# Kernel optimization log

Measured on AMD Instinct MI355X. Metric: run time of the kernel, lower is better.

## Reference

```python
import jax, jax.numpy as jnp
import numpy as np

D = 8        # num_decoders
N = 65536    # num_entries
LAT = 64     # latent_dim
HID = 128    # hidden_dim_dec
FEAT = 16    # feature_dim


def setup_inputs() -> dict:
    key = jax.random.key(0)
    ks = jax.random.split(key, 6)
    return {
        "weight": jax.random.normal(ks[0], (N, LAT), jnp.float32) * 2.0,
        "alpha_param": jax.random.normal(ks[1], (D, N), jnp.float32),  # alpha_std=1.0
        "div": jnp.ones((LAT,), jnp.float32),
        "scale0": jax.random.normal(ks[2], (D, LAT, HID), jnp.float32),  # ldec_std=1.0 normal init
        "shift0": jnp.zeros((D, 1, HID), jnp.float32),
        "scale1": jax.random.normal(ks[3], (D, HID, HID), jnp.float32),
        "shift1": jnp.zeros((D, 1, HID), jnp.float32),
        "scale2": jax.random.normal(ks[4], (D, HID, FEAT), jnp.float32),
        "shift2": jnp.zeros((D, 1, FEAT), jnp.float32),
    }


def _st_round(x):
    # StraightThrough: round in forward, identity gradient
    return x + jax.lax.stop_gradient(jnp.round(x) - x)


def _layer(x, alpha, scale, shift):
    # x: [N, I], alpha: [D, N], scale: [D, I, O], shift: [D, 1, O]
    out = jnp.einsum('ni,dio->dno', x, scale)           # per-decoder GEMMs [D,N,O]
    mix = jnp.einsum('dno,dn->no', out, alpha)          # alpha-weighted combine
    # second alpha-weighted sum over (mix + per-decoder shift), as in the torch code
    return jnp.einsum('dno,dn->no', mix[None, :, :] + shift, alpha)


def reference(weight, alpha_param, div, scale0, shift0, scale1, shift1, scale2, shift2):
    temperature = 1.0
    a = jax.nn.softmax(alpha_param / temperature, axis=0)       # [D, N]
    idx = jnp.argmax(a, axis=0)                                 # [N]
    onehot = jax.nn.one_hot(idx, a.shape[0], dtype=a.dtype).T   # [D, N]
    alpha = a + jax.lax.stop_gradient(onehot - a)               # straight-through one-hot

    x = _st_round(weight) / div                                 # [N, LAT]
    x = jax.nn.relu(_layer(x, alpha, scale0, shift0))           # [N, HID]
    x = jax.nn.relu(_layer(x, alpha, scale1, shift1))           # [N, HID]
    out = _layer(x, alpha, scale2, shift2)                      # [N, FEAT], final_activation='none'
    return out
```

## Files before the change

### kernel.cpp

```cpp
#include <hip/hip_runtime.h>

#define NN 65536
#define DD 8
#define LATD 64
#define HIDD 128
#define FEATD 16
#define BPD 96
#define SXS 72
#define SHS 136

typedef __attribute__((ext_vector_type(8))) short short8;
typedef __attribute__((ext_vector_type(4))) float f32x4;
typedef __attribute__((ext_vector_type(8))) unsigned short ushort8;

static __device__ __forceinline__ unsigned short f2bf(float f) {
  union { float f; unsigned u; } v; v.f = f;
  unsigned r = v.u + 0x7FFFu + ((v.u >> 16) & 1u);
  return (unsigned short)(r >> 16);
}

__global__ __launch_bounds__(256) void k_prep(
    const float* __restrict__ ap, int* __restrict__ cursor,
    unsigned short* __restrict__ perm,
    const float* __restrict__ s0, const float* __restrict__ s1,
    const float* __restrict__ s2,
    unsigned short* __restrict__ g0, unsigned short* __restrict__ g1,
    unsigned short* __restrict__ g2) {
  int bid = blockIdx.x;
  int t = threadIdx.x;
  if (bid < 256) {
    __shared__ int bc[DD];
    __shared__ int bbase[DD];
    if (t < DD) bc[t] = 0;
    __syncthreads();
    int n = bid * 256 + t;
    float best = ap[n];
    int bd = 0;
#pragma unroll
    for (int d = 1; d < DD; ++d) {
      float v = ap[d * NN + n];
      if (v > best) { best = v; bd = d; }
    }
    int lr = atomicAdd(&bc[bd], 1);
    __syncthreads();
    if (t < DD) bbase[t] = atomicAdd(&cursor[t], bc[t]);
    __syncthreads();
    perm[bd * NN + bbase[bd] + lr] = (unsigned short)n;
  } else {
    int o = (bid - 256) * 256 + t;
    if (o < DD * HIDD * LATD) {
      int d = o >> 13, rem = o & 8191, n = rem >> 6, k = rem & 63;
      g0[o] = f2bf(s0[d * 8192 + k * 128 + n]);
    }
    if (o < DD * HIDD * HIDD) {
      int d = o >> 14, rem = o & 16383, n = rem >> 7, k = rem & 127;
      g1[o] = f2bf(s1[d * 16384 + k * 128 + n]);
    }
    if (o < DD * FEATD * HIDD) {
      int d = o >> 11, rem = o & 2047, n = rem >> 7, k = rem & 127;
      g2[o] = f2bf(s2[d * 2048 + k * 16 + n]);
    }
  }
}

__global__ __launch_bounds__(256, 3) void k_mlp(
    const float* __restrict__ weight, const float* __restrict__ divv,
    const unsigned short* __restrict__ g0, const float* __restrict__ sh0,
    const unsigned short* __restrict__ g1, const float* __restrict__ sh1,
    const unsigned short* __restrict__ g2, const float* __restrict__ sh2,
    const int* __restrict__ cursor, const unsigned short* __restrict__ perm,
    float* __restrict__ out) {
  __shared__ unsigned short sX[64 * SXS];
  __shared__ unsigned short sH1[64 * SHS];
  __shared__ unsigned short sH2[64 * SHS];
  __shared__ unsigned short sP[64];

  int d = blockIdx.x / BPD, bslot = blockIdx.x % BPD;
  int cnt = cursor[d];
  int t = threadIdx.x;
  int w = t >> 6, l = t & 63;
  int lrow = l & 15, kgrp = l >> 4;

  short8 b0[2][2];
  short8 b1[2][4];
  short8 b2[4];
  float sh0v[2], sh1v[2];
  const unsigned short* G0 = g0 + d * (HIDD * LATD);
  const unsigned short* G1 = g1 + d * (HIDD * HIDD);
  const unsigned short* G2 = g2 + d * (FEATD * HIDD);
#pragma unroll
  for (int cb = 0; cb < 2; ++cb) {
    int n = (2 * w + cb) * 16 + lrow;
#pragma unroll
    for (int ks = 0; ks < 2; ++ks)
      b0[cb][ks] = *(const short8*)&G0[n * LATD + ks * 32 + kgrp * 8];
#pragma unroll
    for (int ks = 0; ks < 4; ++ks)
      b1[cb][ks] = *(const short8*)&G1[n * HIDD + ks * 32 + kgrp * 8];
    sh0v[cb] = sh0[d * HIDD + n];
    sh1v[cb] = sh1[d * HIDD + n];
  }
#pragma unroll
  for (int ks = 0; ks < 4; ++ks)
    b2[ks] = *(const short8*)&G2[lrow * HIDD + ks * 32 + kgrp * 8];
  float sh2v = sh2[d * FEATD + lrow];

  for (int tile = bslot; tile * 64 < cnt; tile += BPD) {
    int base = tile * 64;

    {
      int r = t >> 2, c = t & 3;
      int gp = base + r;
      unsigned short pe = 0;
      short8 lo = {0, 0, 0, 0, 0, 0, 0, 0}, hi = {0, 0, 0, 0, 0, 0, 0, 0};
      if (gp < cnt) {
        pe = perm[d * NN + gp];
        const float* wr = weight + (int)pe * LATD + c * 16;
        const float* dv = divv + c * 16;
#pragma unroll
        for (int q = 0; q < 2; ++q) {
          float4 f = *(const float4*)(wr + q * 4);
          float4 g = *(const float4*)(dv + q * 4);
          lo[q * 4 + 0] = (short)f2bf(rintf(f.x) / g.x);
          lo[q * 4 + 1] = (short)f2bf(rintf(f.y) / g.y);
          lo[q * 4 + 2] = (short)f2bf(rintf(f.z) / g.z);
          lo[q * 4 + 3] = (short)f2bf(rintf(f.w) / g.w);
        }
#pragma unroll
        for (int q = 0; q < 2; ++q) {
          float4 f = *(const float4*)(wr + 8 + q * 4);
          float4 g = *(const float4*)(dv + 8 + q * 4);
          hi[q * 4 + 0] = (short)f2bf(rintf(f.x) / g.x);
          hi[q * 4 + 1] = (short)f2bf(rintf(f.y) / g.y);
          hi[q * 4 + 2] = (short)f2bf(rintf(f.z) / g.z);
          hi[q * 4 + 3] = (short)f2bf(rintf(f.w) / g.w);
        }
      }
      if (c == 0) sP[r] = pe;
      *(short8*)&sX[r * SXS + c * 16] = lo;
      *(short8*)&sX[r * SXS + c * 16 + 8] = hi;
    }
    __syncthreads();

    int prow[4];
#pragma unroll
    for (int rr = 0; rr < 4; ++rr) prow[rr] = (int)sP[w * 16 + kgrp * 4 + rr];

#pragma unroll
    for (int rg = 0; rg < 4; ++rg) {
      short8 a0 = *(short8*)&sX[(rg * 16 + lrow) * SXS + kgrp * 8];
      short8 a1 = *(short8*)&sX[(rg * 16 + lrow) * SXS + 32 + kgrp * 8];
      __builtin_amdgcn_s_setprio(1);
#pragma unroll
      for (int cb = 0; cb < 2; ++cb) {
        f32x4 acc = {sh0v[cb], sh0v[cb], sh0v[cb], sh0v[cb]};
        acc = __builtin_amdgcn_mfma_f32_16x16x32_bf16(a0, b0[cb][0], acc, 0, 0, 0);
        acc = __builtin_amdgcn_mfma_f32_16x16x32_bf16(a1, b0[cb][1], acc, 0, 0, 0);
#pragma unroll
        for (int rr = 0; rr < 4; ++rr)
          sH1[(rg * 16 + kgrp * 4 + rr) * SHS + (2 * w + cb) * 16 + lrow] =
              f2bf(fmaxf(acc[rr], 0.f));
      }
      __builtin_amdgcn_s_setprio(0);
    }
    __syncthreads();

#pragma unroll
    for (int rg = 0; rg < 4; ++rg) {
      short8 h0 = *(short8*)&sH1[(rg * 16 + lrow) * SHS + kgrp * 8];
      short8 h1 = *(short8*)&sH1[(rg * 16 + lrow) * SHS + 32 + kgrp * 8];
      short8 h2 = *(short8*)&sH1[(rg * 16 + lrow) * SHS + 64 + kgrp * 8];
      short8 h3 = *(short8*)&sH1[(rg * 16 + lrow) * SHS + 96 + kgrp * 8];
      __builtin_amdgcn_s_setprio(1);
#pragma unroll
      for (int cb = 0; cb < 2; ++cb) {
        f32x4 acc = {sh1v[cb], sh1v[cb], sh1v[cb], sh1v[cb]};
        acc = __builtin_amdgcn_mfma_f32_16x16x32_bf16(h0, b1[cb][0], acc, 0, 0, 0);
        acc = __builtin_amdgcn_mfma_f32_16x16x32_bf16(h1, b1[cb][1], acc, 0, 0, 0);
        acc = __builtin_amdgcn_mfma_f32_16x16x32_bf16(h2, b1[cb][2], acc, 0, 0, 0);
        acc = __builtin_amdgcn_mfma_f32_16x16x32_bf16(h3, b1[cb][3], acc, 0, 0, 0);
#pragma unroll
        for (int rr = 0; rr < 4; ++rr)
          sH2[(rg * 16 + kgrp * 4 + rr) * SHS + (2 * w + cb) * 16 + lrow] =
              f2bf(fmaxf(acc[rr], 0.f));
      }
      __builtin_amdgcn_s_setprio(0);
    }
    __syncthreads();

    {
      short8 q0 = *(short8*)&sH2[(w * 16 + lrow) * SHS + kgrp * 8];
      short8 q1 = *(short8*)&sH2[(w * 16 + lrow) * SHS + 32 + kgrp * 8];
      short8 q2 = *(short8*)&sH2[(w * 16 + lrow) * SHS + 64 + kgrp * 8];
      short8 q3 = *(short8*)&sH2[(w * 16 + lrow) * SHS + 96 + kgrp * 8];
      f32x4 acc = {sh2v, sh2v, sh2v, sh2v};
      __builtin_amdgcn_s_setprio(1);
      acc = __builtin_amdgcn_mfma_f32_16x16x32_bf16(q0, b2[0], acc, 0, 0, 0);
      acc = __builtin_amdgcn_mfma_f32_16x16x32_bf16(q1, b2[1], acc, 0, 0, 0);
      acc = __builtin_amdgcn_mfma_f32_16x16x32_bf16(q2, b2[2], acc, 0, 0, 0);
      acc = __builtin_amdgcn_mfma_f32_16x16x32_bf16(q3, b2[3], acc, 0, 0, 0);
      __builtin_amdgcn_s_setprio(0);
#pragma unroll
      for (int rr = 0; rr < 4; ++rr) {
        int row = w * 16 + kgrp * 4 + rr;
        if (base + row < cnt) out[prow[rr] * FEATD + lrow] = acc[rr];
      }
    }
  }
}

extern "C" void kernel_launch(void* const* d_in, const int* in_sizes, int n_in,
                              void* d_out, int out_size, void* d_ws, size_t ws_size,
                              hipStream_t stream) {
  const float* weight      = (const float*)d_in[0];
  const float* alpha_param = (const float*)d_in[1];
  const float* divv        = (const float*)d_in[2];
  const float* scale0      = (const float*)d_in[3];
  const float* shift0      = (const float*)d_in[4];
  const float* scale1      = (const float*)d_in[5];
  const float* shift1      = (const float*)d_in[6];
  const float* scale2      = (const float*)d_in[7];
  const float* shift2      = (const float*)d_in[8];
  float* out = (float*)d_out;

  int* cursor = (int*)d_ws;
  unsigned short* perm = (unsigned short*)((int*)d_ws + 8);
  unsigned short* g0 = perm + DD * NN;
  unsigned short* g1 = g0 + DD * HIDD * LATD;
  unsigned short* g2 = g1 + DD * HIDD * HIDD;

  hipMemsetAsync(cursor, 0, DD * sizeof(int), stream);
  k_prep<<<256 + 512, 256, 0, stream>>>(alpha_param, cursor, perm,
                                        scale0, scale1, scale2, g0, g1, g2);
  k_mlp<<<DD * BPD, 256, 0, stream>>>(weight, divv,
                                      g0, shift0, g1, shift1, g2, shift2,
                                      cursor, perm, out);
}
```

Baseline: 31.45 us.

## Replace argmax-bucketing with single-pass masked per-decoder MFMA over contiguous row tiles

Removes the argmax/permutation pass, the cursor memset and the gathered row access. Each block now takes 64 contiguous rows, computes argmax locally, and runs all 8 decoders' MFMAs with the A operand zeroed for rows that do not belong to each decoder. It also replaces the division by div with a multiply by a precomputed reciprocal. This saves one pass and one launch but issues 8x more MFMA work and reloads decoder weights per block instead of keeping them in registers.

```diff
diff --git a/kernel.cpp b/kernel.cpp
--- a/kernel.cpp
+++ b/kernel.cpp
@@ -5,13 +5,11 @@
 #define LATD 64
 #define HIDD 128
 #define FEATD 16
-#define BPD 96
 #define SXS 72
 #define SHS 136
 
 typedef __attribute__((ext_vector_type(8))) short short8;
 typedef __attribute__((ext_vector_type(4))) float f32x4;
-typedef __attribute__((ext_vector_type(8))) unsigned short ushort8;
 
 static __device__ __forceinline__ unsigned short f2bf(float f) {
   union { float f; unsigned u; } v; v.f = f;
@@ -19,193 +17,215 @@
   return (unsigned short)(r >> 16);
 }
 
+static __device__ __forceinline__ short8 msk(short8 v, bool p) {
+  short8 z = {0, 0, 0, 0, 0, 0, 0, 0};
+  return p ? v : z;
+}
+
 __global__ __launch_bounds__(256) void k_prep(
-    const float* __restrict__ ap, int* __restrict__ cursor,
-    unsigned short* __restrict__ perm,
     const float* __restrict__ s0, const float* __restrict__ s1,
-    const float* __restrict__ s2,
+    const float* __restrict__ s2, const float* __restrict__ divv,
     unsigned short* __restrict__ g0, unsigned short* __restrict__ g1,
-    unsigned short* __restrict__ g2) {
-  int bid = blockIdx.x;
-  int t = threadIdx.x;
-  if (bid < 256) {
-    __shared__ int bc[DD];
-    __shared__ int bbase[DD];
-    if (t < DD) bc[t] = 0;
-    __syncthreads();
-    int n = bid * 256 + t;
-    float best = ap[n];
-    int bd = 0;
-#pragma unroll
-    for (int d = 1; d < DD; ++d) {
-      float v = ap[d * NN + n];
-      if (v > best) { best = v; bd = d; }
-    }
-    int lr = atomicAdd(&bc[bd], 1);
-    __syncthreads();
-    if (t < DD) bbase[t] = atomicAdd(&cursor[t], bc[t]);
-    __syncthreads();
-    perm[bd * NN + bbase[bd] + lr] = (unsigned short)n;
-  } else {
-    int o = (bid - 256) * 256 + t;
-    if (o < DD * HIDD * LATD) {
-      int d = o >> 13, rem = o & 8191, n = rem >> 6, k = rem & 63;
-      g0[o] = f2bf(s0[d * 8192 + k * 128 + n]);
-    }
-    if (o < DD * HIDD * HIDD) {
-      int d = o >> 14, rem = o & 16383, n = rem >> 7, k = rem & 127;
-      g1[o] = f2bf(s1[d * 16384 + k * 128 + n]);
-    }
-    if (o < DD * FEATD * HIDD) {
-      int d = o >> 11, rem = o & 2047, n = rem >> 7, k = rem & 127;
-      g2[o] = f2bf(s2[d * 2048 + k * 16 + n]);
-    }
-  }
-}
-
-__global__ __launch_bounds__(256, 3) void k_mlp(
-    const float* __restrict__ weight, const float* __restrict__ divv,
+    unsigned short* __restrict__ g2, float* __restrict__ rdiv) {
+  int o = blockIdx.x * 256 + threadIdx.x;
+  if (o < DD * HIDD * LATD) {
+    int d = o >> 13, rem = o & 8191, n = rem >> 6, k = rem & 63;
+    g0[o] = f2bf(s0[d * 8192 + k * 128 + n]);
+  }
+  if (o < DD * HIDD * HIDD) {
+    int d = o >> 14, rem = o & 16383, n = rem >> 7, k = rem & 127;
+    g1[o] = f2bf(s1[d * 16384 + k * 128 + n]);
+  }
+  if (o < DD * FEATD * HIDD) {
+    int d = o >> 11, rem = o & 2047, n = rem >> 7, k = rem & 127;
+    g2[o] = f2bf(s2[d * 2048 + k * 16 + n]);
+  }
+  if (o < LATD) rdiv[o] = 1.0f / divv[o];
+}
+
+__global__ __launch_bounds__(256, 3) void k_onepass(
+    const float* __restrict__ weight, const float* __restrict__ ap,
+    const float* __restrict__ rdiv,
     const unsigned short* __restrict__ g0, const float* __restrict__ sh0,
     const unsigned short* __restrict__ g1, const float* __restrict__ sh1,
     const unsigned short* __restrict__ g2, const float* __restrict__ sh2,
-    const int* __restrict__ cursor, const unsigned short* __restrict__ perm,
     float* __restrict__ out) {
   __shared__ unsigned short sX[64 * SXS];
   __shared__ unsigned short sH1[64 * SHS];
   __shared__ unsigned short sH2[64 * SHS];
-  __shared__ unsigned short sP[64];
-
-  int d = blockIdx.x / BPD, bslot = blockIdx.x % BPD;
-  int cnt = cursor[d];
+  __shared__ unsigned char sIdx[64];
+
+  int base = blockIdx.x * 64;
   int t = threadIdx.x;
   int w = t >> 6, l = t & 63;
   int lrow = l & 15, kgrp = l >> 4;
 
-  short8 b0[2][2];
-  short8 b1[2][4];
-  short8 b2[4];
-  float sh0v[2], sh1v[2];
-  const unsigned short* G0 = g0 + d * (HIDD * LATD);
-  const unsigned short* G1 = g1 + d * (HIDD * HIDD);
-  const unsigned short* G2 = g2 + d * (FEATD * HIDD);
-#pragma unroll
-  for (int cb = 0; cb < 2; ++cb) {
-    int n = (2 * w + cb) * 16 + lrow;
-#pragma unroll
-    for (int ks = 0; ks < 2; ++ks)
-      b0[cb][ks] = *(const short8*)&G0[n * LATD + ks * 32 + kgrp * 8];
-#pragma unroll
-    for (int ks = 0; ks < 4; ++ks)
-      b1[cb][ks] = *(const short8*)&G1[n * HIDD + ks * 32 + kgrp * 8];
-    sh0v[cb] = sh0[d * HIDD + n];
-    sh1v[cb] = sh1[d * HIDD + n];
-  }
-#pragma unroll
-  for (int ks = 0; ks < 4; ++ks)
-    b2[ks] = *(const short8*)&G2[lrow * HIDD + ks * 32 + kgrp * 8];
-  float sh2v = sh2[d * FEATD + lrow];
-
-  for (int tile = bslot; tile * 64 < cnt; tile += BPD) {
-    int base = tile * 64;
-
-    {
-      int r = t >> 2, c = t & 3;
-      int gp = base + r;
-      unsigned short pe = 0;
-      short8 lo = {0, 0, 0, 0, 0, 0, 0, 0}, hi = {0, 0, 0, 0, 0, 0, 0, 0};
-      if (gp < cnt) {
-        pe = perm[d * NN + gp];
-        const float* wr = weight + (int)pe * LATD + c * 16;
-        const float* dv = divv + c * 16;
-#pragma unroll
-        for (int q = 0; q < 2; ++q) {
-          float4 f = *(const float4*)(wr + q * 4);
-          float4 g = *(const float4*)(dv + q * 4);
-          lo[q * 4 + 0] = (short)f2bf(rintf(f.x) / g.x);
-          lo[q * 4 + 1] = (short)f2bf(rintf(f.y) / g.y);
-          lo[q * 4 + 2] = (short)f2bf(rintf(f.z) / g.z);
-          lo[q * 4 + 3] = (short)f2bf(rintf(f.w) / g.w);
-        }
-#pragma unroll
-        for (int q = 0; q < 2; ++q) {
-          float4 f = *(const float4*)(wr + 8 + q * 4);
-          float4 g = *(const float4*)(dv + 8 + q * 4);
-          hi[q * 4 + 0] = (short)f2bf(rintf(f.x) / g.x);
-          hi[q * 4 + 1] = (short)f2bf(rintf(f.y) / g.y);
-          hi[q * 4 + 2] = (short)f2bf(rintf(f.z) / g.z);
-          hi[q * 4 + 3] = (short)f2bf(rintf(f.w) / g.w);
+  if (t < 64) {
+    int n = base + t;
+    float best = ap[n];
+    int bd = 0;
+#pragma unroll
+    for (int d = 1; d < DD; ++d) {
+      float v = ap[d * NN + n];
+      if (v > best) { best = v; bd = d; }
+    }
+    sIdx[t] = (unsigned char)bd;
+  }
+
+  {
+    int r = t >> 2, c = t & 3;
+    const float* wr = weight + (base + r) * LATD + c * 16;
+    const float* rd = rdiv + c * 16;
+    short8 lo8, hi8;
+#pragma unroll
+    for (int q = 0; q < 2; ++q) {
+      float4 f = *(const float4*)(wr + q * 4);
+      float4 g = *(const float4*)(rd + q * 4);
+      lo8[q * 4 + 0] = (short)f2bf(rintf(f.x) * g.x);
+      lo8[q * 4 + 1] = (short)f2bf(rintf(f.y) * g.y);
+      lo8[q * 4 + 2] = (short)f2bf(rintf(f.z) * g.z);
+      lo8[q * 4 + 3] = (short)f2bf(rintf(f.w) * g.w);
+    }
+#pragma unroll
+    for (int q = 0; q < 2; ++q) {
+      float4 f = *(const float4*)(wr + 8 + q * 4);
+      float4 g = *(const float4*)(rd + 8 + q * 4);
+      hi8[q * 4 + 0] = (short)f2bf(rintf(f.x) * g.x);
+      hi8[q * 4 + 1] = (short)f2bf(rintf(f.y) * g.y);
+      hi8[q * 4 + 2] = (short)f2bf(rintf(f.z) * g.z);
+      hi8[q * 4 + 3] = (short)f2bf(rintf(f.w) * g.w);
+    }
+    *(short8*)&sX[r * SXS + c * 16] = lo8;
+    *(short8*)&sX[r * SXS + c * 16 + 8] = hi8;
+  }
+  __syncthreads();
+
+  int arow[4], dec16[4][4];
+#pragma unroll
+  for (int rg = 0; rg < 4; ++rg) {
+    arow[rg] = sIdx[rg * 16 + lrow];
+#pragma unroll
+    for (int rr = 0; rr < 4; ++rr) dec16[rg][rr] = sIdx[rg * 16 + kgrp * 4 + rr];
+  }
+
+  short8 xa[4][2];
+#pragma unroll
+  for (int rg = 0; rg < 4; ++rg) {
+    xa[rg][0] = *(short8*)&sX[(rg * 16 + lrow) * SXS + kgrp * 8];
+    xa[rg][1] = *(short8*)&sX[(rg * 16 + lrow) * SXS + 32 + kgrp * 8];
+  }
+  {
+    f32x4 acc[4][2];
+#pragma unroll
+    for (int rg = 0; rg < 4; ++rg)
+#pragma unroll
+      for (int cb = 0; cb < 2; ++cb)
+#pragma unroll
+        for (int rr = 0; rr < 4; ++rr)
+          acc[rg][cb][rr] = sh0[dec16[rg][rr] * HIDD + (2 * w + cb) * 16 + lrow];
+
+    for (int d = 0; d < DD; ++d) {
+      const unsigned short* G0 = g0 + d * (HIDD * LATD);
+      short8 b[2][2];
+#pragma unroll
+      for (int cb = 0; cb < 2; ++cb)
+#pragma unroll
+        for (int ks = 0; ks < 2; ++ks)
+          b[cb][ks] = *(const short8*)&G0[((2 * w + cb) * 16 + lrow) * LATD + ks * 32 + kgrp * 8];
+#pragma unroll
+      for (int rg = 0; rg < 4; ++rg) {
+        bool p = (arow[rg] == d);
+        short8 a0 = msk(xa[rg][0], p), a1 = msk(xa[rg][1], p);
+#pragma unroll
+        for (int cb = 0; cb < 2; ++cb) {
+          acc[rg][cb] = __builtin_amdgcn_mfma_f32_16x16x32_bf16(a0, b[cb][0], acc[rg][cb], 0, 0, 0);
+          acc[rg][cb] = __builtin_amdgcn_mfma_f32_16x16x32_bf16(a1, b[cb][1], acc[rg][cb], 0, 0, 0);
         }
       }
-      if (c == 0) sP[r] = pe;
-      *(short8*)&sX[r * SXS + c * 16] = lo;
-      *(short8*)&sX[r * SXS + c * 16 + 8] = hi;
-    }
-    __syncthreads();
-
-    int prow[4];
-#pragma unroll
-    for (int rr = 0; rr < 4; ++rr) prow[rr] = (int)sP[w * 16 + kgrp * 4 + rr];
-
-#pragma unroll
-    for (int rg = 0; rg < 4; ++rg) {
-      short8 a0 = *(short8*)&sX[(rg * 16 + lrow) * SXS + kgrp * 8];
-      short8 a1 = *(short8*)&sX[(rg * 16 + lrow) * SXS + 32 + kgrp * 8];
-      __builtin_amdgcn_s_setprio(1);
-#pragma unroll
-      for (int cb = 0; cb < 2; ++cb) {
-        f32x4 acc = {sh0v[cb], sh0v[cb], sh0v[cb], sh0v[cb]};
-        acc = __builtin_amdgcn_mfma_f32_16x16x32_bf16(a0, b0[cb][0], acc, 0, 0, 0);
-        acc = __builtin_amdgcn_mfma_f32_16x16x32_bf16(a1, b0[cb][1], acc, 0, 0, 0);
+    }
+#pragma unroll
+    for (int rg = 0; rg < 4; ++rg)
+#pragma unroll
+      for (int cb = 0; cb < 2; ++cb)
 #pragma unroll
         for (int rr = 0; rr < 4; ++rr)
           sH1[(rg * 16 + kgrp * 4 + rr) * SHS + (2 * w + cb) * 16 + lrow] =
-              f2bf(fmaxf(acc[rr], 0.f));
+              f2bf(fmaxf(acc[rg][cb][rr], 0.f));
+  }
+  __syncthreads();
+
+  {
+    short8 ha[4][4];
+#pragma unroll
+    for (int rg = 0; rg < 4; ++rg)
+#pragma unroll
+      for (int s = 0; s < 4; ++s)
+        ha[rg][s] = *(short8*)&sH1[(rg * 16 + lrow) * SHS + s * 32 + kgrp * 8];
+
+    f32x4 acc[4][2];
+#pragma unroll
+    for (int rg = 0; rg < 4; ++rg)
+#pragma unroll
+      for (int cb = 0; cb < 2; ++cb)
+#pragma unroll
+        for (int rr = 0; rr < 4; ++rr)
+          acc[rg][cb][rr] = sh1[dec16[rg][rr] * HIDD + (2 * w + cb) * 16 + lrow];
+
+    for (int d = 0; d < DD; ++d) {
+      const unsigned short* G1 = g1 + d * (HIDD * HIDD);
+      short8 b[2][4];
+#pragma unroll
+      for (int cb = 0; cb < 2; ++cb)
+#pragma unroll
+        for (int ks = 0; ks < 4; ++ks)
+          b[cb][ks] = *(const short8*)&G1[((2 * w + cb) * 16 + lrow) * HIDD + ks * 32 + kgrp * 8];
+#pragma unroll
+      for (int rg = 0; rg < 4; ++rg) {
+        bool p = (arow[rg] == d);
+#pragma unroll
+        for (int cb = 0; cb < 2; ++cb) {
+#pragma unroll
+          for (int s = 0; s < 4; ++s)
+            acc[rg][cb] = __builtin_amdgcn_mfma_f32_16x16x32_bf16(msk(ha[rg][s], p), b[cb][s], acc[rg][cb], 0, 0, 0);
+        }
       }
-      __builtin_amdgcn_s_setprio(0);
-    }
-    __syncthreads();
-
-#pragma unroll
-    for (int rg = 0; rg < 4; ++rg) {
-      short8 h0 = *(short8*)&sH1[(rg * 16 + lrow) * SHS + kgrp * 8];
-      short8 h1 = *(short8*)&sH1[(rg * 16 + lrow) * SHS + 32 + kgrp * 8];
-      short8 h2 = *(short8*)&sH1[(rg * 16 + lrow) * SHS + 64 + kgrp * 8];
-      short8 h3 = *(short8*)&sH1[(rg * 16 + lrow) * SHS + 96 + kgrp * 8];
-      __builtin_amdgcn_s_setprio(1);
-#pragma unroll
-      for (int cb = 0; cb < 2; ++cb) {
-        f32x4 acc = {sh1v[cb], sh1v[cb], sh1v[cb], sh1v[cb]};
-        acc = __builtin_amdgcn_mfma_f32_16x16x32_bf16(h0, b1[cb][0], acc, 0, 0, 0);
-        acc = __builtin_amdgcn_mfma_f32_16x16x32_bf16(h1, b1[cb][1], acc, 0, 0, 0);
-        acc = __builtin_amdgcn_mfma_f32_16x16x32_bf16(h2, b1[cb][2], acc, 0, 0, 0);
-        acc = __builtin_amdgcn_mfma_f32_16x16x32_bf16(h3, b1[cb][3], acc, 0, 0, 0);
+    }
+#pragma unroll
+    for (int rg = 0; rg < 4; ++rg)
+#pragma unroll
+      for (int cb = 0; cb < 2; ++cb)
 #pragma unroll
         for (int rr = 0; rr < 4; ++rr)
           sH2[(rg * 16 + kgrp * 4 + rr) * SHS + (2 * w + cb) * 16 + lrow] =
-              f2bf(fmaxf(acc[rr], 0.f));
-      }
-      __builtin_amdgcn_s_setprio(0);
-    }
-    __syncthreads();
-
-    {
-      short8 q0 = *(short8*)&sH2[(w * 16 + lrow) * SHS + kgrp * 8];
-      short8 q1 = *(short8*)&sH2[(w * 16 + lrow) * SHS + 32 + kgrp * 8];
-      short8 q2 = *(short8*)&sH2[(w * 16 + lrow) * SHS + 64 + kgrp * 8];
-      short8 q3 = *(short8*)&sH2[(w * 16 + lrow) * SHS + 96 + kgrp * 8];
-      f32x4 acc = {sh2v, sh2v, sh2v, sh2v};
-      __builtin_amdgcn_s_setprio(1);
-      acc = __builtin_amdgcn_mfma_f32_16x16x32_bf16(q0, b2[0], acc, 0, 0, 0);
-      acc = __builtin_amdgcn_mfma_f32_16x16x32_bf16(q1, b2[1], acc, 0, 0, 0);
-      acc = __builtin_amdgcn_mfma_f32_16x16x32_bf16(q2, b2[2], acc, 0, 0, 0);
-      acc = __builtin_amdgcn_mfma_f32_16x16x32_bf16(q3, b2[3], acc, 0, 0, 0);
-      __builtin_amdgcn_s_setprio(0);
-#pragma unroll
-      for (int rr = 0; rr < 4; ++rr) {
-        int row = w * 16 + kgrp * 4 + rr;
-        if (base + row < cnt) out[prow[rr] * FEATD + lrow] = acc[rr];
-      }
-    }
+              f2bf(fmaxf(acc[rg][cb][rr], 0.f));
+  }
+  __syncthreads();
+
+  {
+    short8 qa[4];
+#pragma unroll
+    for (int s = 0; s < 4; ++s)
+      qa[s] = *(short8*)&sH2[(w * 16 + lrow) * SHS + s * 32 + kgrp * 8];
+    int a3 = sIdx[w * 16 + lrow];
+    f32x4 acc;
+#pragma unroll
+    for (int rr = 0; rr < 4; ++rr)
+      acc[rr] = sh2[sIdx[w * 16 + kgrp * 4 + rr] * FEATD + lrow];
+
+    for (int d = 0; d < DD; ++d) {
+      const unsigned short* G2 = g2 + d * (FEATD * HIDD);
+      short8 b[4];
+#pragma unroll
+      for (int ks = 0; ks < 4; ++ks)
+        b[ks] = *(const short8*)&G2[lrow * HIDD + ks * 32 + kgrp * 8];
+      bool p = (a3 == d);
+#pragma unroll
+      for (int ks = 0; ks < 4; ++ks)
+        acc = __builtin_amdgcn_mfma_f32_16x16x32_bf16(msk(qa[ks], p), b[ks], acc, 0, 0, 0);
+    }
+#pragma unroll
+    for (int rr = 0; rr < 4; ++rr)
+      out[(base + w * 16 + kgrp * 4 + rr) * FEATD + lrow] = acc[rr];
   }
 }
 
@@ -223,16 +243,12 @@
   const float* shift2      = (const float*)d_in[8];
   float* out = (float*)d_out;
 
-  int* cursor = (int*)d_ws;
-  unsigned short* perm = (unsigned short*)((int*)d_ws + 8);
-  unsigned short* g0 = perm + DD * NN;
+  float* rdiv = (float*)d_ws;
+  unsigned short* g0 = (unsigned short*)(rdiv + 64);
   unsigned short* g1 = g0 + DD * HIDD * LATD;
   unsigned short* g2 = g1 + DD * HIDD * HIDD;
 
-  hipMemsetAsync(cursor, 0, DD * sizeof(int), stream);
-  k_prep<<<256 + 512, 256, 0, stream>>>(alpha_param, cursor, perm,
-                                        scale0, scale1, scale2, g0, g1, g2);
-  k_mlp<<<DD * BPD, 256, 0, stream>>>(weight, divv,
-                                      g0, shift0, g1, shift1, g2, shift2,
-                                      cursor, perm, out);
-}
+  k_prep<<<512, 256, 0, stream>>>(scale0, scale1, scale2, divv, g0, g1, g2, rdiv);
+  k_onepass<<<NN / 64, 256, 0, stream>>>(weight, alpha_param, rdiv,
+                                         g0, shift0, g1, shift1, g2, shift2, out);
+}
```

Result: slower. 87.05 us (+176.8%).

## Halve MLP row tile, double blocks per decoder, precompute reciprocal divisor

Applied to the files above, without the earlier changes.

Shrinks the per-block row tile from 64 to 32 rows and doubles the number of blocks per decoder, raising the occupancy hint from 3 to 6 blocks per CU. This aims at more latency hiding and better load balance for the gather-heavy MLP. The per-element division by div becomes a multiply by a reciprocal precomputed in the prep kernel, and the s_setprio hints are removed. In exchange, weight fragments are reloaded by twice as many blocks, and in the last layer only half the waves do MFMA work.

```diff
diff --git a/kernel.cpp b/kernel.cpp
--- a/kernel.cpp
+++ b/kernel.cpp
@@ -5,13 +5,13 @@
 #define LATD 64
 #define HIDD 128
 #define FEATD 16
-#define BPD 96
+#define BPD 192
+#define TILE 32
 #define SXS 72
 #define SHS 136
 
 typedef __attribute__((ext_vector_type(8))) short short8;
 typedef __attribute__((ext_vector_type(4))) float f32x4;
-typedef __attribute__((ext_vector_type(8))) unsigned short ushort8;
 
 static __device__ __forceinline__ unsigned short f2bf(float f) {
   union { float f; unsigned u; } v; v.f = f;
@@ -23,9 +23,9 @@
     const float* __restrict__ ap, int* __restrict__ cursor,
     unsigned short* __restrict__ perm,
     const float* __restrict__ s0, const float* __restrict__ s1,
-    const float* __restrict__ s2,
+    const float* __restrict__ s2, const float* __restrict__ divv,
     unsigned short* __restrict__ g0, unsigned short* __restrict__ g1,
-    unsigned short* __restrict__ g2) {
+    unsigned short* __restrict__ g2, float* __restrict__ rdiv) {
   int bid = blockIdx.x;
   int t = threadIdx.x;
   if (bid < 256) {
@@ -60,20 +60,21 @@
       int d = o >> 11, rem = o & 2047, n = rem >> 7, k = rem & 127;
       g2[o] = f2bf(s2[d * 2048 + k * 16 + n]);
     }
+    if (o < LATD) rdiv[o] = 1.0f / divv[o];
   }
 }
 
-__global__ __launch_bounds__(256, 3) void k_mlp(
-    const float* __restrict__ weight, const float* __restrict__ divv,
+__global__ __launch_bounds__(256, 6) void k_mlp(
+    const float* __restrict__ weight, const float* __restrict__ rdiv,
     const unsigned short* __restrict__ g0, const float* __restrict__ sh0,
     const unsigned short* __restrict__ g1, const float* __restrict__ sh1,
     const unsigned short* __restrict__ g2, const float* __restrict__ sh2,
     const int* __restrict__ cursor, const unsigned short* __restrict__ perm,
     float* __restrict__ out) {
-  __shared__ unsigned short sX[64 * SXS];
-  __shared__ unsigned short sH1[64 * SHS];
-  __shared__ unsigned short sH2[64 * SHS];
-  __shared__ unsigned short sP[64];
+  __shared__ unsigned short sX[TILE * SXS];
+  __shared__ unsigned short sH1[TILE * SHS];
+  __shared__ unsigned short sH2[TILE * SHS];
+  __shared__ unsigned short sP[TILE];
 
   int d = blockIdx.x / BPD, bslot = blockIdx.x % BPD;
   int cnt = cursor[d];
@@ -85,72 +86,68 @@
   short8 b1[2][4];
   short8 b2[4];
   float sh0v[2], sh1v[2];
-  const unsigned short* G0 = g0 + d * (HIDD * LATD);
-  const unsigned short* G1 = g1 + d * (HIDD * HIDD);
-  const unsigned short* G2 = g2 + d * (FEATD * HIDD);
-#pragma unroll
-  for (int cb = 0; cb < 2; ++cb) {
-    int n = (2 * w + cb) * 16 + lrow;
-#pragma unroll
-    for (int ks = 0; ks < 2; ++ks)
-      b0[cb][ks] = *(const short8*)&G0[n * LATD + ks * 32 + kgrp * 8];
+  {
+    const unsigned short* G0 = g0 + d * (HIDD * LATD);
+    const unsigned short* G1 = g1 + d * (HIDD * HIDD);
+    const unsigned short* G2 = g2 + d * (FEATD * HIDD);
+#pragma unroll
+    for (int cb = 0; cb < 2; ++cb) {
+      int n2 = (2 * w + cb) * 16 + lrow;
+#pragma unroll
+      for (int ks = 0; ks < 2; ++ks)
+        b0[cb][ks] = *(const short8*)&G0[n2 * LATD + ks * 32 + kgrp * 8];
+#pragma unroll
+      for (int ks = 0; ks < 4; ++ks)
+        b1[cb][ks] = *(const short8*)&G1[n2 * HIDD + ks * 32 + kgrp * 8];
+      sh0v[cb] = sh0[d * HIDD + n2];
+      sh1v[cb] = sh1[d * HIDD + n2];
+    }
 #pragma unroll
     for (int ks = 0; ks < 4; ++ks)
-      b1[cb][ks] = *(const short8*)&G1[n * HIDD + ks * 32 + kgrp * 8];
-    sh0v[cb] = sh0[d * HIDD + n];
-    sh1v[cb] = sh1[d * HIDD + n];
+      b2[ks] = *(const short8*)&G2[lrow * HIDD + ks * 32 + kgrp * 8];
   }
-#pragma unroll
-  for (int ks = 0; ks < 4; ++ks)
-    b2[ks] = *(const short8*)&G2[lrow * HIDD + ks * 32 + kgrp * 8];
   float sh2v = sh2[d * FEATD + lrow];
 
-  for (int tile = bslot; tile * 64 < cnt; tile += BPD) {
-    int base = tile * 64;
+  for (int tile = bslot; tile * TILE < cnt; tile += BPD) {
+    int base = tile * TILE;
 
     {
-      int r = t >> 2, c = t & 3;
+      int r = t >> 3, c = t & 7;
       int gp = base + r;
       unsigned short pe = 0;
-      short8 lo = {0, 0, 0, 0, 0, 0, 0, 0}, hi = {0, 0, 0, 0, 0, 0, 0, 0};
+      short8 v8 = {0, 0, 0, 0, 0, 0, 0, 0};
       if (gp < cnt) {
         pe = perm[d * NN + gp];
-        const float* wr = weight + (int)pe * LATD + c * 16;
-        const float* dv = divv + c * 16;
-#pragma unroll
-        for (int q = 0; q < 2; ++q) {
-          float4 f = *(const float4*)(wr + q * 4);
-          float4 g = *(const float4*)(dv + q * 4);
-          lo[q * 4 + 0] = (short)f2bf(rintf(f.x) / g.x);
-          lo[q * 4 + 1] = (short)f2bf(rintf(f.y) / g.y);
-          lo[q * 4 + 2] = (short)f2bf(rintf(f.z) / g.z);
-          lo[q * 4 + 3] = (short)f2bf(rintf(f.w) / g.w);
-        }
-#pragma unroll
-        for (int q = 0; q < 2; ++q) {
-          float4 f = *(const float4*)(wr + 8 + q * 4);
-          float4 g = *(const float4*)(dv + 8 + q * 4);
-          hi[q * 4 + 0] = (short)f2bf(rintf(f.x) / g.x);
-          hi[q * 4 + 1] = (short)f2bf(rintf(f.y) / g.y);
-          hi[q * 4 + 2] = (short)f2bf(rintf(f.z) / g.z);
-          hi[q * 4 + 3] = (short)f2bf(rintf(f.w) / g.w);
-        }
+        const float* wr = weight + (int)pe * LATD + c * 8;
+        const float* rd = rdiv + c * 8;
+        float4 f0 = *(const float4*)wr;
+        float4 f1 = *(const float4*)(wr + 4);
+        float4 q0 = *(const float4*)rd;
+        float4 q1 = *(const float4*)(rd + 4);
+        v8[0] = (short)f2bf(rintf(f0.x) * q0.x);
+        v8[1] = (short)f2bf(rintf(f0.y) * q0.y);
+        v8[2] = (short)f2bf(rintf(f0.z) * q0.z);
+        v8[3] = (short)f2bf(rintf(f0.w) * q0.w);
+        v8[4] = (short)f2bf(rintf(f1.x) * q1.x);
+        v8[5] = (short)f2bf(rintf(f1.y) * q1.y);
+        v8[6] = (short)f2bf(rintf(f1.z) * q1.z);
+        v8[7] = (short)f2bf(rintf(f1.w) * q1.w);
       }
       if (c == 0) sP[r] = pe;
-      *(short8*)&sX[r * SXS + c * 16] = lo;
-      *(short8*)&sX[r * SXS + c * 16 + 8] = hi;
-    }
-    __syncthreads();
-
-    int prow[4];
-#pragma unroll
-    for (int rr = 0; rr < 4; ++rr) prow[rr] = (int)sP[w * 16 + kgrp * 4 + rr];
-
-#pragma unroll
-    for (int rg = 0; rg < 4; ++rg) {
+      *(short8*)&sX[r * SXS + c * 8] = v8;
+    }
+    __syncthreads();
+
+    int prow[4] = {0, 0, 0, 0};
+    if (w < 2) {
+#pragma unroll
+      for (int rr = 0; rr < 4; ++rr) prow[rr] = (int)sP[w * 16 + kgrp * 4 + rr];
+    }
+
+#pragma unroll
+    for (int rg = 0; rg < 2; ++rg) {
       short8 a0 = *(short8*)&sX[(rg * 16 + lrow) * SXS + kgrp * 8];
       short8 a1 = *(short8*)&sX[(rg * 16 + lrow) * SXS + 32 + kgrp * 8];
-      __builtin_amdgcn_s_setprio(1);
 #pragma unroll
       for (int cb = 0; cb < 2; ++cb) {
         f32x4 acc = {sh0v[cb], sh0v[cb], sh0v[cb], sh0v[cb]};
@@ -161,17 +158,15 @@
           sH1[(rg * 16 + kgrp * 4 + rr) * SHS + (2 * w + cb) * 16 + lrow] =
               f2bf(fmaxf(acc[rr], 0.f));
       }
-      __builtin_amdgcn_s_setprio(0);
-    }
-    __syncthreads();
-
-#pragma unroll
-    for (int rg = 0; rg < 4; ++rg) {
+    }
+    __syncthreads();
+
+#pragma unroll
+    for (int rg = 0; rg < 2; ++rg) {
       short8 h0 = *(short8*)&sH1[(rg * 16 + lrow) * SHS + kgrp * 8];
       short8 h1 = *(short8*)&sH1[(rg * 16 + lrow) * SHS + 32 + kgrp * 8];
       short8 h2 = *(short8*)&sH1[(rg * 16 + lrow) * SHS + 64 + kgrp * 8];
       short8 h3 = *(short8*)&sH1[(rg * 16 + lrow) * SHS + 96 + kgrp * 8];
-      __builtin_amdgcn_s_setprio(1);
 #pragma unroll
       for (int cb = 0; cb < 2; ++cb) {
         f32x4 acc = {sh1v[cb], sh1v[cb], sh1v[cb], sh1v[cb]};
@@ -184,22 +179,19 @@
           sH2[(rg * 16 + kgrp * 4 + rr) * SHS + (2 * w + cb) * 16 + lrow] =
               f2bf(fmaxf(acc[rr], 0.f));
       }
-      __builtin_amdgcn_s_setprio(0);
-    }
-    __syncthreads();
-
-    {
+    }
+    __syncthreads();
+
+    if (w < 2) {
       short8 q0 = *(short8*)&sH2[(w * 16 + lrow) * SHS + kgrp * 8];
       short8 q1 = *(short8*)&sH2[(w * 16 + lrow) * SHS + 32 + kgrp * 8];
       short8 q2 = *(short8*)&sH2[(w * 16 + lrow) * SHS + 64 + kgrp * 8];
       short8 q3 = *(short8*)&sH2[(w * 16 + lrow) * SHS + 96 + kgrp * 8];
       f32x4 acc = {sh2v, sh2v, sh2v, sh2v};
-      __builtin_amdgcn_s_setprio(1);
       acc = __builtin_amdgcn_mfma_f32_16x16x32_bf16(q0, b2[0], acc, 0, 0, 0);
       acc = __builtin_amdgcn_mfma_f32_16x16x32_bf16(q1, b2[1], acc, 0, 0, 0);
       acc = __builtin_amdgcn_mfma_f32_16x16x32_bf16(q2, b2[2], acc, 0, 0, 0);
       acc = __builtin_amdgcn_mfma_f32_16x16x32_bf16(q3, b2[3], acc, 0, 0, 0);
-      __builtin_amdgcn_s_setprio(0);
 #pragma unroll
       for (int rr = 0; rr < 4; ++rr) {
         int row = w * 16 + kgrp * 4 + rr;
@@ -224,15 +216,17 @@
   float* out = (float*)d_out;
 
   int* cursor = (int*)d_ws;
-  unsigned short* perm = (unsigned short*)((int*)d_ws + 8);
+  float* rdiv = (float*)(cursor + 16);
+  unsigned short* perm = (unsigned short*)(rdiv + 64);
   unsigned short* g0 = perm + DD * NN;
   unsigned short* g1 = g0 + DD * HIDD * LATD;
   unsigned short* g2 = g1 + DD * HIDD * HIDD;
 
   hipMemsetAsync(cursor, 0, DD * sizeof(int), stream);
-  k_prep<<<256 + 512, 256, 0, stream>>>(alpha_param, cursor, perm,
-                                        scale0, scale1, scale2, g0, g1, g2);
-  k_mlp<<<DD * BPD, 256, 0, stream>>>(weight, divv,
+  k_prep<<<768, 256, 0, stream>>>(alpha_param, cursor, perm,
+                                  scale0, scale1, scale2, divv,
+                                  g0, g1, g2, rdiv);
+  k_mlp<<<DD * BPD, 256, 0, stream>>>(weight, rdiv,
                                       g0, shift0, g1, shift1, g2, shift2,
                                       cursor, perm, out);
 }
```

Result: slower. 70.25 us (+123.4%).

## Add separate gather kernel producing contiguous bf16 inputs sorted by decoder

Applied to the files above, without the earlier changes.

Adds a k_gather kernel that, after routing, writes each entry's rounded and scaled weight row as bf16 into a workspace buffer in decoder-sorted order. The MLP kernel can then load contiguous tiles instead of scattered fp32 rows. It also replaces the per-element division with a precomputed reciprocal of div, drops the setprio hints, and reads output row indices straight from perm instead of shared memory. The cost is an extra kernel launch plus a full 8 MB write and read pass over global memory, and the gather path only runs when the workspace is large enough.

```diff
diff --git a/kernel.cpp b/kernel.cpp
--- a/kernel.cpp
+++ b/kernel.cpp
@@ -11,7 +11,6 @@
 
 typedef __attribute__((ext_vector_type(8))) short short8;
 typedef __attribute__((ext_vector_type(4))) float f32x4;
-typedef __attribute__((ext_vector_type(8))) unsigned short ushort8;
 
 static __device__ __forceinline__ unsigned short f2bf(float f) {
   union { float f; unsigned u; } v; v.f = f;
@@ -23,9 +22,9 @@
     const float* __restrict__ ap, int* __restrict__ cursor,
     unsigned short* __restrict__ perm,
     const float* __restrict__ s0, const float* __restrict__ s1,
-    const float* __restrict__ s2,
+    const float* __restrict__ s2, const float* __restrict__ divv,
     unsigned short* __restrict__ g0, unsigned short* __restrict__ g1,
-    unsigned short* __restrict__ g2) {
+    unsigned short* __restrict__ g2, float* __restrict__ rdiv) {
   int bid = blockIdx.x;
   int t = threadIdx.x;
   if (bid < 256) {
@@ -60,97 +59,143 @@
       int d = o >> 11, rem = o & 2047, n = rem >> 7, k = rem & 127;
       g2[o] = f2bf(s2[d * 2048 + k * 16 + n]);
     }
+    if (o < LATD) rdiv[o] = 1.0f / divv[o];
+  }
+}
+
+__global__ __launch_bounds__(256) void k_gather(
+    const float* __restrict__ weight, const float* __restrict__ rdiv,
+    const int* __restrict__ cursor, const unsigned short* __restrict__ perm,
+    unsigned short* __restrict__ gx) {
+  int e = blockIdx.x * 256 + threadIdx.x;
+  int off = 0, d = 0, acc = 0;
+#pragma unroll
+  for (int k = 0; k < DD - 1; ++k) {
+    acc += cursor[k];
+    if (e >= acc) { d = k + 1; off = acc; }
+  }
+  int entry = (int)perm[d * NN + (e - off)];
+  const float* wr = weight + (size_t)entry * LATD;
+  unsigned short* gr = gx + (size_t)e * LATD;
+#pragma unroll
+  for (int q = 0; q < 16; ++q) {
+    float4 f = *(const float4*)(wr + q * 4);
+    float4 g = *(const float4*)(rdiv + q * 4);
+    unsigned short o0 = f2bf(rintf(f.x) * g.x);
+    unsigned short o1 = f2bf(rintf(f.y) * g.y);
+    unsigned short o2 = f2bf(rintf(f.z) * g.z);
+    unsigned short o3 = f2bf(rintf(f.w) * g.w);
+    *(ushort2*)(gr + q * 4) = make_ushort2(o0, o1);
+    *(ushort2*)(gr + q * 4 + 2) = make_ushort2(o2, o3);
   }
 }
 
 __global__ __launch_bounds__(256, 3) void k_mlp(
-    const float* __restrict__ weight, const float* __restrict__ divv,
+    const float* __restrict__ weight, const float* __restrict__ rdiv,
     const unsigned short* __restrict__ g0, const float* __restrict__ sh0,
     const unsigned short* __restrict__ g1, const float* __restrict__ sh1,
     const unsigned short* __restrict__ g2, const float* __restrict__ sh2,
     const int* __restrict__ cursor, const unsigned short* __restrict__ perm,
+    const unsigned short* __restrict__ gx, int use_gx,
     float* __restrict__ out) {
   __shared__ unsigned short sX[64 * SXS];
   __shared__ unsigned short sH1[64 * SHS];
   __shared__ unsigned short sH2[64 * SHS];
-  __shared__ unsigned short sP[64];
 
   int d = blockIdx.x / BPD, bslot = blockIdx.x % BPD;
-  int cnt = cursor[d];
   int t = threadIdx.x;
   int w = t >> 6, l = t & 63;
   int lrow = l & 15, kgrp = l >> 4;
+
+  int cnt = cursor[d];
+  int offd = 0;
+#pragma unroll
+  for (int k = 0; k < DD - 1; ++k)
+    if (k < d) offd += cursor[k];
 
   short8 b0[2][2];
   short8 b1[2][4];
   short8 b2[4];
   float sh0v[2], sh1v[2];
-  const unsigned short* G0 = g0 + d * (HIDD * LATD);
-  const unsigned short* G1 = g1 + d * (HIDD * HIDD);
-  const unsigned short* G2 = g2 + d * (FEATD * HIDD);
-#pragma unroll
-  for (int cb = 0; cb < 2; ++cb) {
-    int n = (2 * w + cb) * 16 + lrow;
-#pragma unroll
-    for (int ks = 0; ks < 2; ++ks)
-      b0[cb][ks] = *(const short8*)&G0[n * LATD + ks * 32 + kgrp * 8];
+  {
+    const unsigned short* G0 = g0 + d * (HIDD * LATD);
+    const unsigned short* G1 = g1 + d * (HIDD * HIDD);
+    const unsigned short* G2 = g2 + d * (FEATD * HIDD);
+#pragma unroll
+    for (int cb = 0; cb < 2; ++cb) {
+      int n2 = (2 * w + cb) * 16 + lrow;
+#pragma unroll
+      for (int ks = 0; ks < 2; ++ks)
+        b0[cb][ks] = *(const short8*)&G0[n2 * LATD + ks * 32 + kgrp * 8];
+#pragma unroll
+      for (int ks = 0; ks < 4; ++ks)
+        b1[cb][ks] = *(const short8*)&G1[n2 * HIDD + ks * 32 + kgrp * 8];
+      sh0v[cb] = sh0[d * HIDD + n2];
+      sh1v[cb] = sh1[d * HIDD + n2];
+    }
 #pragma unroll
     for (int ks = 0; ks < 4; ++ks)
-      b1[cb][ks] = *(const short8*)&G1[n * HIDD + ks * 32 + kgrp * 8];
-    sh0v[cb] = sh0[d * HIDD + n];
-    sh1v[cb] = sh1[d * HIDD + n];
-  }
-#pragma unroll
-  for (int ks = 0; ks < 4; ++ks)
-    b2[ks] = *(const short8*)&G2[lrow * HIDD + ks * 32 + kgrp * 8];
+      b2[ks] = *(const short8*)&G2[lrow * HIDD + ks * 32 + kgrp * 8];
+  }
   float sh2v = sh2[d * FEATD + lrow];
 
   for (int tile = bslot; tile * 64 < cnt; tile += BPD) {
     int base = tile * 64;
 
-    {
+    if (use_gx) {
       int r = t >> 2, c = t & 3;
       int gp = base + r;
-      unsigned short pe = 0;
+      short8 v0 = {0, 0, 0, 0, 0, 0, 0, 0}, v1 = {0, 0, 0, 0, 0, 0, 0, 0};
+      if (gp < cnt) {
+        const unsigned short* gr = gx + (size_t)(offd + gp) * LATD + c * 16;
+        v0 = *(const short8*)gr;
+        v1 = *(const short8*)(gr + 8);
+      }
+      *(short8*)&sX[r * SXS + c * 16] = v0;
+      *(short8*)&sX[r * SXS + c * 16 + 8] = v1;
+    } else {
+      int r = t >> 2, c = t & 3;
+      int gp = base + r;
       short8 lo = {0, 0, 0, 0, 0, 0, 0, 0}, hi = {0, 0, 0, 0, 0, 0, 0, 0};
       if (gp < cnt) {
-        pe = perm[d * NN + gp];
-        const float* wr = weight + (int)pe * LATD + c * 16;
-        const float* dv = divv + c * 16;
+        int pe = (int)perm[d * NN + gp];
+        const float* wr = weight + (size_t)pe * LATD + c * 16;
+        const float* rd = rdiv + c * 16;
 #pragma unroll
         for (int q = 0; q < 2; ++q) {
           float4 f = *(const float4*)(wr + q * 4);
-          float4 g = *(const float4*)(dv + q * 4);
-          lo[q * 4 + 0] = (short)f2bf(rintf(f.x) / g.x);
-          lo[q * 4 + 1] = (short)f2bf(rintf(f.y) / g.y);
-          lo[q * 4 + 2] = (short)f2bf(rintf(f.z) / g.z);
-          lo[q * 4 + 3] = (short)f2bf(rintf(f.w) / g.w);
+          float4 g = *(const float4*)(rd + q * 4);
+          lo[q * 4 + 0] = (short)f2bf(rintf(f.x) * g.x);
+          lo[q * 4 + 1] = (short)f2bf(rintf(f.y) * g.y);
+          lo[q * 4 + 2] = (short)f2bf(rintf(f.z) * g.z);
+          lo[q * 4 + 3] = (short)f2bf(rintf(f.w) * g.w);
         }
 #pragma unroll
         for (int q = 0; q < 2; ++q) {
           float4 f = *(const float4*)(wr + 8 + q * 4);
-          float4 g = *(const float4*)(dv + 8 + q * 4);
-          hi[q * 4 + 0] = (short)f2bf(rintf(f.x) / g.x);
-          hi[q * 4 + 1] = (short)f2bf(rintf(f.y) / g.y);
-          hi[q * 4 + 2] = (short)f2bf(rintf(f.z) / g.z);
-          hi[q * 4 + 3] = (short)f2bf(rintf(f.w) / g.w);
+          float4 g = *(const float4*)(rd + 8 + q * 4);
+          hi[q * 4 + 0] = (short)f2bf(rintf(f.x) * g.x);
+          hi[q * 4 + 1] = (short)f2bf(rintf(f.y) * g.y);
+          hi[q * 4 + 2] = (short)f2bf(rintf(f.z) * g.z);
+          hi[q * 4 + 3] = (short)f2bf(rintf(f.w) * g.w);
         }
       }
-      if (c == 0) sP[r] = pe;
       *(short8*)&sX[r * SXS + c * 16] = lo;
       *(short8*)&sX[r * SXS + c * 16 + 8] = hi;
     }
-    __syncthreads();
 
     int prow[4];
 #pragma unroll
-    for (int rr = 0; rr < 4; ++rr) prow[rr] = (int)sP[w * 16 + kgrp * 4 + rr];
+    for (int rr = 0; rr < 4; ++rr) {
+      int row = w * 16 + kgrp * 4 + rr;
+      prow[rr] = (base + row < cnt) ? (int)perm[d * NN + base + row] : 0;
+    }
+    __syncthreads();
 
 #pragma unroll
     for (int rg = 0; rg < 4; ++rg) {
       short8 a0 = *(short8*)&sX[(rg * 16 + lrow) * SXS + kgrp * 8];
       short8 a1 = *(short8*)&sX[(rg * 16 + lrow) * SXS + 32 + kgrp * 8];
-      __builtin_amdgcn_s_setprio(1);
 #pragma unroll
       for (int cb = 0; cb < 2; ++cb) {
         f32x4 acc = {sh0v[cb], sh0v[cb], sh0v[cb], sh0v[cb]};
@@ -161,7 +206,6 @@
           sH1[(rg * 16 + kgrp * 4 + rr) * SHS + (2 * w + cb) * 16 + lrow] =
               f2bf(fmaxf(acc[rr], 0.f));
       }
-      __builtin_amdgcn_s_setprio(0);
     }
     __syncthreads();
 
@@ -171,7 +215,6 @@
       short8 h1 = *(short8*)&sH1[(rg * 16 + lrow) * SHS + 32 + kgrp * 8];
       short8 h2 = *(short8*)&sH1[(rg * 16 + lrow) * SHS + 64 + kgrp * 8];
       short8 h3 = *(short8*)&sH1[(rg * 16 + lrow) * SHS + 96 + kgrp * 8];
-      __builtin_amdgcn_s_setprio(1);
 #pragma unroll
       for (int cb = 0; cb < 2; ++cb) {
         f32x4 acc = {sh1v[cb], sh1v[cb], sh1v[cb], sh1v[cb]};
@@ -184,7 +227,6 @@
           sH2[(rg * 16 + kgrp * 4 + rr) * SHS + (2 * w + cb) * 16 + lrow] =
               f2bf(fmaxf(acc[rr], 0.f));
       }
-      __builtin_amdgcn_s_setprio(0);
     }
     __syncthreads();
 
@@ -194,18 +236,17 @@
       short8 q2 = *(short8*)&sH2[(w * 16 + lrow) * SHS + 64 + kgrp * 8];
       short8 q3 = *(short8*)&sH2[(w * 16 + lrow) * SHS + 96 + kgrp * 8];
       f32x4 acc = {sh2v, sh2v, sh2v, sh2v};
-      __builtin_amdgcn_s_setprio(1);
       acc = __builtin_amdgcn_mfma_f32_16x16x32_bf16(q0, b2[0], acc, 0, 0, 0);
       acc = __builtin_amdgcn_mfma_f32_16x16x32_bf16(q1, b2[1], acc, 0, 0, 0);
       acc = __builtin_amdgcn_mfma_f32_16x16x32_bf16(q2, b2[2], acc, 0, 0, 0);
       acc = __builtin_amdgcn_mfma_f32_16x16x32_bf16(q3, b2[3], acc, 0, 0, 0);
-      __builtin_amdgcn_s_setprio(0);
 #pragma unroll
       for (int rr = 0; rr < 4; ++rr) {
         int row = w * 16 + kgrp * 4 + rr;
         if (base + row < cnt) out[prow[rr] * FEATD + lrow] = acc[rr];
       }
     }
+    __syncthreads();
   }
 }
 
@@ -223,16 +264,24 @@
   const float* shift2      = (const float*)d_in[8];
   float* out = (float*)d_out;
 
-  int* cursor = (int*)d_ws;
-  unsigned short* perm = (unsigned short*)((int*)d_ws + 8);
-  unsigned short* g0 = perm + DD * NN;
-  unsigned short* g1 = g0 + DD * HIDD * LATD;
-  unsigned short* g2 = g1 + DD * HIDD * HIDD;
+  char* ws = (char*)d_ws;
+  int* cursor          = (int*)ws;
+  float* rdiv          = (float*)(ws + 256);
+  unsigned short* perm = (unsigned short*)(ws + 512);
+  unsigned short* g0   = perm + DD * NN;
+  unsigned short* g1   = g0 + DD * HIDD * LATD;
+  unsigned short* g2   = g1 + DD * HIDD * HIDD;
+  unsigned short* gx   = g2 + DD * FEATD * HIDD;
+  size_t need = (size_t)((char*)(gx + (size_t)NN * LATD) - ws);
+  int use_gx = (ws_size >= need) ? 1 : 0;
 
   hipMemsetAsync(cursor, 0, DD * sizeof(int), stream);
-  k_prep<<<256 + 512, 256, 0, stream>>>(alpha_param, cursor, perm,
-                                        scale0, scale1, scale2, g0, g1, g2);
-  k_mlp<<<DD * BPD, 256, 0, stream>>>(weight, divv,
+  k_prep<<<768, 256, 0, stream>>>(alpha_param, cursor, perm,
+                                  scale0, scale1, scale2, divv,
+                                  g0, g1, g2, rdiv);
+  if (use_gx)
+    k_gather<<<NN / 256, 256, 0, stream>>>(weight, rdiv, cursor, perm, gx);
+  k_mlp<<<DD * BPD, 256, 0, stream>>>(weight, rdiv,
                                       g0, shift0, g1, shift1, g2, shift2,
-                                      cursor, perm, out);
-}
+                                      cursor, perm, gx, use_gx, out);
+}
```

Measured after the change: 38.07 us. +21.0%, slower.
